# Kernel optimization log

Measured on AMD Instinct MI355X. Metric: run time of the kernel, lower is better.

## Reference

```python
import jax, jax.numpy as jnp
import numpy as np

B, S, D, H = 2, 2048, 1024, 16
DK = D // H

def setup_inputs() -> dict:
    key = jax.random.key(0)
    ks = jax.random.split(key, 12)
    scale = 1.0 / np.sqrt(D)
    inp = {
        'q': jax.random.normal(ks[0], (B, S, D), jnp.float32),
        'k': jax.random.normal(ks[1], (B, S, D), jnp.float32),
        'v': jax.random.normal(ks[2], (B, S, D), jnp.float32),
        # causal mask: 1 where attending is allowed (j <= i), 0 for future tokens
        'mask': jnp.tril(jnp.ones((S, S), jnp.int32))[None, None, :, :],
        'wq': jax.random.normal(ks[3], (D, D), jnp.float32) * scale,
        'bq': jnp.zeros((D,), jnp.float32),
        'wk': jax.random.normal(ks[4], (D, D), jnp.float32) * scale,
        'bk': jnp.zeros((D,), jnp.float32),
        'wv': jax.random.normal(ks[5], (D, D), jnp.float32) * scale,
        'bv': jnp.zeros((D,), jnp.float32),
        'wo': jax.random.normal(ks[6], (D, D), jnp.float32) * scale,
        'bo': jnp.zeros((D,), jnp.float32),
    }
    return inp


def reference(q, k, v, mask, wq, bq, wk, bk, wv, bv, wo, bo):
    def split_heads(x):
        # [B,S,D] -> [B,H,S,DK]
        return x.reshape(B, S, H, DK).transpose(0, 2, 1, 3)

    query = split_heads(q @ wq + bq)
    key_ = split_heads(k @ wk + bk)
    value = split_heads(v @ wv + bv)

    # [B,H,S,S] attention scores
    scores = jnp.einsum('bhqd,bhkd->bhqk', query, key_) / jnp.sqrt(
        jnp.asarray(DK, jnp.float32))
    scores = jnp.where(mask == 0, jnp.asarray(-1e9, scores.dtype), scores)
    attn = jax.nn.softmax(scores, axis=-1)  # dropout p=0.0 (eval mode)

    x = jnp.einsum('bhqk,bhkd->bhqd', attn, value)  # [B,H,S,DK]
    x = x.transpose(0, 2, 1, 3).reshape(B, S, D)
    return x @ wo + bo
```

## Files before the change

### kernel.cpp

```cpp
#include <hip/hip_runtime.h>
#include <hip/hip_bf16.h>

#define BATCH 2
#define SEQ   2048
#define DMODEL 1024
#define NHEAD 16
#define DK    64
#define MTOK  (BATCH * SEQ)

typedef __attribute__((ext_vector_type(8))) short bf16x8;
typedef __attribute__((ext_vector_type(4))) float f32x4;

__device__ __forceinline__ unsigned short f2bf(float x) {
    unsigned u = __float_as_uint(x);
    u = (u + 0x7FFFu + ((u >> 16) & 1u)) >> 16;
    return (unsigned short)u;
}

__device__ __forceinline__ void store_out(float* p, float v)          { *p = v; }
__device__ __forceinline__ void store_out(unsigned short* p, float v) { *p = f2bf(v); }

__device__ __forceinline__ void g2lds16(const void* g, void* l) {
    __builtin_amdgcn_global_load_lds(
        (const __attribute__((address_space(1))) void*)g,
        (__attribute__((address_space(3))) void*)l, 16, 0, 0);
}

template <int N>
__device__ __forceinline__ void s_wait_vmcnt() {
    asm volatile("s_waitcnt vmcnt(%0)" :: "n"(N) : "memory");
}
__device__ __forceinline__ void s_wait_lgkm0() {
    asm volatile("s_waitcnt lgkmcnt(0)" ::: "memory");
}
__device__ __forceinline__ void s_bar() {
    asm volatile("s_barrier" ::: "memory");
}

__global__ __launch_bounds__(256) void cvt3_bf16_kernel(
    const float* __restrict__ s0, const float* __restrict__ s1,
    const float* __restrict__ s2,
    unsigned short* __restrict__ d0, unsigned short* __restrict__ d1,
    unsigned short* __restrict__ d2, int n)
{
    const float* src; unsigned short* dst;
    switch (blockIdx.z) {
        case 0:  src = s0; dst = d0; break;
        case 1:  src = s1; dst = d1; break;
        default: src = s2; dst = d2; break;
    }
    int i = (blockIdx.x * 256 + threadIdx.x) * 8;
    if (i >= n) return;
    float4 a = *(const float4*)(src + i);
    float4 b = *(const float4*)(src + i + 4);
    union { unsigned short s[8]; uint4 u; } o;
    o.s[0] = f2bf(a.x); o.s[1] = f2bf(a.y); o.s[2] = f2bf(a.z); o.s[3] = f2bf(a.w);
    o.s[4] = f2bf(b.x); o.s[5] = f2bf(b.y); o.s[6] = f2bf(b.z); o.s[7] = f2bf(b.w);
    *(uint4*)(dst + i) = o.u;
}

__global__ __launch_bounds__(256) void wtrans_kernel(
    const float* __restrict__ w0, const float* __restrict__ w1,
    const float* __restrict__ w2, const float* __restrict__ w3,
    unsigned short* __restrict__ t0, unsigned short* __restrict__ t1,
    unsigned short* __restrict__ t2, unsigned short* __restrict__ t3)
{
    __shared__ float tile[32][33];
    const float* W; unsigned short* T;
    switch (blockIdx.z) {
        case 0:  W = w0; T = t0; break;
        case 1:  W = w1; T = t1; break;
        case 2:  W = w2; T = t2; break;
        default: W = w3; T = t3; break;
    }
    const int n0 = blockIdx.x * 32, k0 = blockIdx.y * 32;
    const int t  = threadIdx.x;
    const int r  = t >> 3;
    const int c4 = (t & 7) * 4;

    float4 v = *(const float4*)&W[(size_t)(k0 + r) * DMODEL + n0 + c4];
    tile[r][c4 + 0] = v.x; tile[r][c4 + 1] = v.y;
    tile[r][c4 + 2] = v.z; tile[r][c4 + 3] = v.w;
    __syncthreads();

    union { unsigned short s[4]; uint2 u; } o;
#pragma unroll
    for (int u = 0; u < 4; ++u) o.s[u] = f2bf(tile[c4 + u][r]);
    *(uint2*)&T[(size_t)(n0 + r) * DMODEL + k0 + c4] = o.u;
}

struct GemmP {
    const unsigned short* A;
    const unsigned short* Bt;
    const float* bias;
    void* C;
    int N, K, ctShift, biasByRow;
    float scale;
};
struct Gemm3 { GemmP p[3]; };

template <typename OutT, int NC>
__global__ __launch_bounds__(512, 2) void gemm_lds_kernel(Gemm3 g)
{
    constexpr int NCW   = NC / 4;
    constexpr int NBLK  = 32 + 2 * NC;
    constexpr int PW    = NBLK / 8;
    constexpr int BUFSZ = NBLK * 512;

    __shared__ unsigned short sS[2 * BUFSZ];

    const unsigned nx  = gridDim.x;
    const unsigned lin = blockIdx.x + nx * blockIdx.z;
    const unsigned ch  = (nx * gridDim.z) >> 3;
    const unsigned l2  = (lin & 7u) * ch + (lin >> 3);
    const unsigned zz  = l2 / nx;
    const unsigned bid = l2 - zz * nx;

    const GemmP p = g.p[zz];
    const unsigned short* __restrict__ A  = p.A;
    const unsigned short* __restrict__ Bt = p.Bt;
    OutT* __restrict__ C = (OutT*)p.C;
    const int K = p.K, N = p.N;

    const int bx = (int)(bid & ((1u << p.ctShift) - 1u));
    const int by = (int)(bid >> p.ctShift);
    const int row0 = by * 256;
    const int col0 = bx * (NC * 16);

    const int t    = threadIdx.x;
    const int w    = t >> 6;
    const int lane = t & 63;
    const int ln   = lane & 15;
    const int qg   = lane >> 4;
    const int wm   = w >> 2;
    const int wn   = w & 3;

    const unsigned short* sp[PW];
    int lo[PW];
#pragma unroll
    for (int i = 0; i < PW; ++i) {
        const int s = w * PW + i;
        if (s < 32) {
            const int mtg = s >> 1, kc = s & 1;
            sp[i] = A + (size_t)(row0 + mtg * 16 + ln) * K + kc * 32 + qg * 8;
        } else {
            const int bi = s - 32;
            const int ntg = bi >> 1, kc = bi & 1;
            sp[i] = Bt + (size_t)(col0 + ntg * 16 + ln) * K + kc * 32 + qg * 8;
        }
        lo[i] = s * 512;
    }

    f32x4 acc[8][NCW];
#pragma unroll
    for (int mt = 0; mt < 8; ++mt)
#pragma unroll
        for (int nt = 0; nt < NCW; ++nt) acc[mt][nt] = (f32x4){0.f, 0.f, 0.f, 0.f};

    const int NT = K / 64;

#pragma unroll
    for (int i = 0; i < PW; ++i) g2lds16(sp[i], &sS[lo[i]]);
#pragma unroll
    for (int i = 0; i < PW; ++i) g2lds16(sp[i] + 64, &sS[BUFSZ + lo[i]]);

    int curOff = 0;
    for (int kt = 0; kt < NT; ++kt) {
        if (kt < NT - 1) s_wait_vmcnt<PW>();
        else             s_wait_vmcnt<0>();
        s_bar();

        const unsigned short* bufA = &sS[curOff];
        const unsigned short* bufB = &sS[curOff + 32 * 512];
#pragma unroll
        for (int kc = 0; kc < 2; ++kc) {
            bf16x8 aF[8], bF[NCW];
#pragma unroll
            for (int mt = 0; mt < 8; ++mt)
                aF[mt] = *(const bf16x8*)&bufA[(((wm * 8 + mt) * 2) + kc) * 512 + lane * 8];
#pragma unroll
            for (int n2 = 0; n2 < NCW; ++n2)
                bF[n2] = *(const bf16x8*)&bufB[(((wn * NCW + n2) * 2) + kc) * 512 + lane * 8];
#pragma unroll
            for (int mt = 0; mt < 8; ++mt)
#pragma unroll
                for (int n2 = 0; n2 < NCW; ++n2)
                    acc[mt][n2] = __builtin_amdgcn_mfma_f32_16x16x32_bf16(
                        aF[mt], bF[n2], acc[mt][n2], 0, 0, 0);
        }

        s_wait_lgkm0();
        s_bar();

        if (kt + 2 < NT) {
            const int koff = (kt + 2) * 64;
#pragma unroll
            for (int i = 0; i < PW; ++i)
                g2lds16(sp[i] + koff, &sS[curOff + lo[i]]);
        }
        curOff ^= BUFSZ;
    }

    float bcol[NCW], brow[8][4];
    if (!p.biasByRow) {
#pragma unroll
        for (int n2 = 0; n2 < NCW; ++n2)
            bcol[n2] = p.bias[col0 + (wn * NCW + n2) * 16 + ln];
    } else {
#pragma unroll
        for (int mt = 0; mt < 8; ++mt)
#pragma unroll
            for (int r = 0; r < 4; ++r)
                brow[mt][r] = p.bias[row0 + wm * 128 + mt * 16 + qg * 4 + r];
    }

#pragma unroll
    for (int mt = 0; mt < 8; ++mt)
#pragma unroll
        for (int n2 = 0; n2 < NCW; ++n2)
#pragma unroll
            for (int r = 0; r < 4; ++r) {
                int row = row0 + wm * 128 + mt * 16 + qg * 4 + r;
                int col = col0 + (wn * NCW + n2) * 16 + ln;
                float bb = p.biasByRow ? brow[mt][r] : bcol[n2];
                store_out(&C[(size_t)row * N + col], (acc[mt][n2][r] + bb) * p.scale);
            }
}

#define BR 64
#define BC 64
#define PSTR 72

__global__ __launch_bounds__(256) void attn_mfma_kernel(
    const unsigned short* __restrict__ Qg, const unsigned short* __restrict__ Kg,
    const unsigned short* __restrict__ VT, unsigned short* __restrict__ O)
{
    __shared__ unsigned short sK[2][8 * 512];
    __shared__ unsigned short sV[2][8 * 512];
    __shared__ unsigned short sQ[8 * 512];
    __shared__ unsigned short sP[BR * PSTR];

    const int t    = threadIdx.x;
    const int w    = t >> 6;
    const int lane = t & 63;
    const int ln   = lane & 15;
    const int qg   = lane >> 4;

    const int id  = blockIdx.x;
    const int bh  = id & 31;
    const int qt  = (SEQ / BR - 1) - (id >> 5);
    const int b   = bh >> 4;
    const int h   = bh & 15;
    const int qi0 = qt * BR;

    const size_t rowbase = (size_t)b * SEQ;
    const size_t colbase = (size_t)h * DK;

#pragma unroll
    for (int i = 0; i < 2; ++i) {
        const int s = w * 2 + i;
        const int nt = s >> 1, kc = s & 1;
        g2lds16(Qg + (rowbase + qi0 + w * 16 + ln) * DMODEL + colbase + i * 32 + qg * 8,
                &sQ[s * 512]);
        g2lds16(Kg + (rowbase + nt * 16 + ln) * DMODEL + colbase + kc * 32 + qg * 8,
                &sK[0][s * 512]);
        g2lds16(VT + (size_t)(colbase + nt * 16 + ln) * MTOK + rowbase + kc * 32 + qg * 8,
                &sV[0][s * 512]);
    }
    __syncthreads();

    bf16x8 aq[2];
#pragma unroll
    for (int kc = 0; kc < 2; ++kc)
        aq[kc] = *(const bf16x8*)&sQ[(w * 2 + kc) * 512 + lane * 8];

    const short one_bf = (short)0x3F80;
    const bf16x8 bone = (bf16x8){one_bf, one_bf, one_bf, one_bf,
                                 one_bf, one_bf, one_bf, one_bf};

    f32x4 ofrag[4];
#pragma unroll
    for (int nt = 0; nt < 4; ++nt) ofrag[nt] = (f32x4){0.f, 0.f, 0.f, 0.f};
    f32x4 osum = (f32x4){0.f, 0.f, 0.f, 0.f};
    float m_r[4];
#pragma unroll
    for (int r = 0; r < 4; ++r) m_r[r] = -3.0e38f;

    const int ntiles = qt + 1;
    for (int jt = 0; jt < ntiles; ++jt) {
        const int cur = jt & 1;

        if (jt + 1 < ntiles) {
            const int j1 = (jt + 1) * BC;
            const int nb = cur ^ 1;
#pragma unroll
            for (int i = 0; i < 2; ++i) {
                const int s = w * 2 + i;
                const int nt = s >> 1, kc = s & 1;
                g2lds16(Kg + (rowbase + j1 + nt * 16 + ln) * DMODEL + colbase + kc * 32 + qg * 8,
                        &sK[nb][s * 512]);
                g2lds16(VT + (size_t)(colbase + nt * 16 + ln) * MTOK + rowbase + j1 + kc * 32 + qg * 8,
                        &sV[nb][s * 512]);
            }
        }

        f32x4 sf[4];
#pragma unroll
        for (int nt = 0; nt < 4; ++nt) {
            f32x4 a2 = (f32x4){0.f, 0.f, 0.f, 0.f};
#pragma unroll
            for (int kc = 0; kc < 2; ++kc) {
                bf16x8 bk = *(const bf16x8*)&sK[cur][(nt * 2 + kc) * 512 + lane * 8];
                a2 = __builtin_amdgcn_mfma_f32_16x16x32_bf16(aq[kc], bk, a2, 0, 0, 0);
            }
            sf[nt] = a2;
        }

        if (jt == ntiles - 1) {
#pragma unroll
            for (int nt = 0; nt < 4; ++nt)
#pragma unroll
                for (int r = 0; r < 4; ++r) {
                    int qrow = w * 16 + qg * 4 + r;
                    int col  = nt * 16 + ln;
                    if (col > qrow) sf[nt][r] = -1.0e30f;
                }
        }

        float rmax[4];
#pragma unroll
        for (int r = 0; r < 4; ++r)
            rmax[r] = fmaxf(fmaxf(sf[0][r], sf[1][r]), fmaxf(sf[2][r], sf[3][r]));
#pragma unroll
        for (int off = 8; off >= 1; off >>= 1)
#pragma unroll
            for (int r = 0; r < 4; ++r)
                rmax[r] = fmaxf(rmax[r], __shfl_xor(rmax[r], off));

        float alpha[4];
#pragma unroll
        for (int r = 0; r < 4; ++r) {
            float mn = fmaxf(m_r[r], rmax[r]);
            alpha[r] = exp2f(m_r[r] - mn);
            m_r[r] = mn;
        }

#pragma unroll
        for (int nt = 0; nt < 4; ++nt)
#pragma unroll
            for (int r = 0; r < 4; ++r) {
                float pv = exp2f(sf[nt][r] - m_r[r]);
                int row = w * 16 + qg * 4 + r;
                int col = (nt * 16 + ln) ^ (((w * 4 + qg) & 7) * 8);
                sP[row * PSTR + col] = f2bf(pv);
            }

#pragma unroll
        for (int nt = 0; nt < 4; ++nt)
#pragma unroll
            for (int r = 0; r < 4; ++r) ofrag[nt][r] *= alpha[r];
#pragma unroll
        for (int r = 0; r < 4; ++r) osum[r] *= alpha[r];

        bf16x8 apf[2];
#pragma unroll
        for (int kc = 0; kc < 2; ++kc) {
            int row = w * 16 + ln;
            int col = (kc * 32 + qg * 8) ^ ((((row >> 2) & 7)) * 8);
            apf[kc] = *(const bf16x8*)&sP[row * PSTR + col];
        }

#pragma unroll
        for (int kc = 0; kc < 2; ++kc)
            osum = __builtin_amdgcn_mfma_f32_16x16x32_bf16(apf[kc], bone, osum, 0, 0, 0);
#pragma unroll
        for (int nt = 0; nt < 4; ++nt) {
#pragma unroll
            for (int kc = 0; kc < 2; ++kc) {
                bf16x8 bv = *(const bf16x8*)&sV[cur][(nt * 2 + kc) * 512 + lane * 8];
                ofrag[nt] = __builtin_amdgcn_mfma_f32_16x16x32_bf16(apf[kc], bv, ofrag[nt], 0, 0, 0);
            }
        }

        __syncthreads();
    }

    float inv[4];
#pragma unroll
    for (int r = 0; r < 4; ++r) inv[r] = 1.0f / osum[r];
#pragma unroll
    for (int nt = 0; nt < 4; ++nt)
#pragma unroll
        for (int r = 0; r < 4; ++r) {
            int gq = qi0 + w * 16 + qg * 4 + r;
            O[(rowbase + gq) * DMODEL + colbase + nt * 16 + ln] =
                f2bf(ofrag[nt][r] * inv[r]);
        }
}

extern "C" void kernel_launch(void* const* d_in, const int* in_sizes, int n_in,
                              void* d_out, int out_size, void* d_ws, size_t ws_size,
                              hipStream_t stream)
{
    const float* q  = (const float*)d_in[0];
    const float* k  = (const float*)d_in[1];
    const float* v  = (const float*)d_in[2];
    const float* wq = (const float*)d_in[4];
    const float* bq = (const float*)d_in[5];
    const float* wk = (const float*)d_in[6];
    const float* bk = (const float*)d_in[7];
    const float* wv = (const float*)d_in[8];
    const float* bv = (const float*)d_in[9];
    const float* wo = (const float*)d_in[10];
    const float* bo = (const float*)d_in[11];
    float* out = (float*)d_out;

    const size_t mat  = (size_t)MTOK * DMODEL;
    const size_t wmat = (size_t)DMODEL * DMODEL;
    unsigned short* Abq = (unsigned short*)d_ws;
    unsigned short* Abk = Abq + mat;
    unsigned short* Abv = Abk + mat;
    unsigned short* WtQ = Abv + mat;
    unsigned short* WtK = WtQ + wmat;
    unsigned short* WtV = WtK + wmat;
    unsigned short* WtO = WtV + wmat;
    unsigned short* Qb  = WtO + wmat;
    unsigned short* Kb  = Qb + mat;
    unsigned short* VT  = Kb + mat;
    unsigned short* CTX = VT + mat;

    cvt3_bf16_kernel<<<dim3((unsigned)(mat / 2048), 1, 3), 256, 0, stream>>>(
        q, k, v, Abq, Abk, Abv, (int)mat);
    wtrans_kernel<<<dim3(32, 32, 4), 256, 0, stream>>>(wq, wk, wv, wo, WtQ, WtK, WtV, WtO);

    const float qscale = 0.125f * 1.44269504088896f;
    Gemm3 g;
    g.p[0] = (GemmP){Abq, WtQ, bq, (void*)Qb, DMODEL, DMODEL, 2, 0, qscale};
    g.p[1] = (GemmP){Abk, WtK, bk, (void*)Kb, DMODEL, DMODEL, 2, 0, 1.0f};
    g.p[2] = (GemmP){WtV, Abv, bv, (void*)VT, MTOK,   DMODEL, 4, 1, 1.0f};
    gemm_lds_kernel<unsigned short, 16><<<dim3(64, 1, 3), 512, 0, stream>>>(g);

    attn_mfma_kernel<<<BATCH * NHEAD * (SEQ / BR), 256, 0, stream>>>(Qb, Kb, VT, CTX);

    Gemm3 go;
    go.p[0] = (GemmP){CTX, WtO, bo, (void*)out, DMODEL, DMODEL, 3, 0, 1.0f};
    go.p[1] = go.p[0];
    go.p[2] = go.p[0];
    gemm_lds_kernel<float, 8><<<dim3(128, 1, 1), 512, 0, stream>>>(go);
}
```

Before: 270.4 us.

## Compute transposed scores to keep P in registers; shrink output GEMM tile

The attention kernel now computes S^T by swapping MFMA operands, so each lane holds a key-column slice for one query row. Row max and sum reduce with two cross-group shuffles, and the P tile is repacked into MFMA A-operand layout with cross-lane shuffles and packed bf16 converts. This removes the shared-memory P buffer, its write/read round trip and the ones-vector MFMA that computed row sums. Separately, the GEMM template gains an M-tile parameter, and the output projection uses 128x128 tiles with 256 blocks to fill more compute units, at the cost of more operand reloads.

Result: faster. 257.1 us (-4.9%).

```diff
diff --git a/kernel.cpp b/kernel.cpp
--- a/kernel.cpp
+++ b/kernel.cpp
@@ -19,6 +19,12 @@
 
 __device__ __forceinline__ void store_out(float* p, float v)          { *p = v; }
 __device__ __forceinline__ void store_out(unsigned short* p, float v) { *p = f2bf(v); }
+
+__device__ __forceinline__ unsigned cvt_pk_bf16(float x, float y) {
+    unsigned d;
+    asm("v_cvt_pk_bf16_f32 %0, %1, %2" : "=v"(d) : "v"(x), "v"(y));
+    return d;
+}
 
 __device__ __forceinline__ void g2lds16(const void* g, void* l) {
     __builtin_amdgcn_global_load_lds(
@@ -99,11 +105,12 @@
 };
 struct Gemm3 { GemmP p[3]; };
 
-template <typename OutT, int NC>
+template <typename OutT, int MR, int NC>
 __global__ __launch_bounds__(512, 2) void gemm_lds_kernel(Gemm3 g)
 {
+    constexpr int AM    = MR / 2;
     constexpr int NCW   = NC / 4;
-    constexpr int NBLK  = 32 + 2 * NC;
+    constexpr int NBLK  = 2 * MR + 2 * NC;
     constexpr int PW    = NBLK / 8;
     constexpr int BUFSZ = NBLK * 512;
 
@@ -124,7 +131,7 @@
 
     const int bx = (int)(bid & ((1u << p.ctShift) - 1u));
     const int by = (int)(bid >> p.ctShift);
-    const int row0 = by * 256;
+    const int row0 = by * (MR * 16);
     const int col0 = bx * (NC * 16);
 
     const int t    = threadIdx.x;
@@ -140,20 +147,20 @@
 #pragma unroll
     for (int i = 0; i < PW; ++i) {
         const int s = w * PW + i;
-        if (s < 32) {
+        if (s < 2 * MR) {
             const int mtg = s >> 1, kc = s & 1;
             sp[i] = A + (size_t)(row0 + mtg * 16 + ln) * K + kc * 32 + qg * 8;
         } else {
-            const int bi = s - 32;
+            const int bi = s - 2 * MR;
             const int ntg = bi >> 1, kc = bi & 1;
             sp[i] = Bt + (size_t)(col0 + ntg * 16 + ln) * K + kc * 32 + qg * 8;
         }
         lo[i] = s * 512;
     }
 
-    f32x4 acc[8][NCW];
-#pragma unroll
-    for (int mt = 0; mt < 8; ++mt)
+    f32x4 acc[AM][NCW];
+#pragma unroll
+    for (int mt = 0; mt < AM; ++mt)
 #pragma unroll
         for (int nt = 0; nt < NCW; ++nt) acc[mt][nt] = (f32x4){0.f, 0.f, 0.f, 0.f};
 
@@ -171,18 +178,18 @@
         s_bar();
 
         const unsigned short* bufA = &sS[curOff];
-        const unsigned short* bufB = &sS[curOff + 32 * 512];
+        const unsigned short* bufB = &sS[curOff + 2 * MR * 512];
 #pragma unroll
         for (int kc = 0; kc < 2; ++kc) {
-            bf16x8 aF[8], bF[NCW];
-#pragma unroll
-            for (int mt = 0; mt < 8; ++mt)
-                aF[mt] = *(const bf16x8*)&bufA[(((wm * 8 + mt) * 2) + kc) * 512 + lane * 8];
+            bf16x8 aF[AM], bF[NCW];
+#pragma unroll
+            for (int mt = 0; mt < AM; ++mt)
+                aF[mt] = *(const bf16x8*)&bufA[(((wm * AM + mt) * 2) + kc) * 512 + lane * 8];
 #pragma unroll
             for (int n2 = 0; n2 < NCW; ++n2)
                 bF[n2] = *(const bf16x8*)&bufB[(((wn * NCW + n2) * 2) + kc) * 512 + lane * 8];
 #pragma unroll
-            for (int mt = 0; mt < 8; ++mt)
+            for (int mt = 0; mt < AM; ++mt)
 #pragma unroll
                 for (int n2 = 0; n2 < NCW; ++n2)
                     acc[mt][n2] = __builtin_amdgcn_mfma_f32_16x16x32_bf16(
@@ -201,26 +208,26 @@
         curOff ^= BUFSZ;
     }
 
-    float bcol[NCW], brow[8][4];
+    float bcol[NCW], brow[AM][4];
     if (!p.biasByRow) {
 #pragma unroll
         for (int n2 = 0; n2 < NCW; ++n2)
             bcol[n2] = p.bias[col0 + (wn * NCW + n2) * 16 + ln];
     } else {
 #pragma unroll
-        for (int mt = 0; mt < 8; ++mt)
+        for (int mt = 0; mt < AM; ++mt)
 #pragma unroll
             for (int r = 0; r < 4; ++r)
-                brow[mt][r] = p.bias[row0 + wm * 128 + mt * 16 + qg * 4 + r];
-    }
-
-#pragma unroll
-    for (int mt = 0; mt < 8; ++mt)
+                brow[mt][r] = p.bias[row0 + wm * (AM * 16) + mt * 16 + qg * 4 + r];
+    }
+
+#pragma unroll
+    for (int mt = 0; mt < AM; ++mt)
 #pragma unroll
         for (int n2 = 0; n2 < NCW; ++n2)
 #pragma unroll
             for (int r = 0; r < 4; ++r) {
-                int row = row0 + wm * 128 + mt * 16 + qg * 4 + r;
+                int row = row0 + wm * (AM * 16) + mt * 16 + qg * 4 + r;
                 int col = col0 + (wn * NCW + n2) * 16 + ln;
                 float bb = p.biasByRow ? brow[mt][r] : bcol[n2];
                 store_out(&C[(size_t)row * N + col], (acc[mt][n2][r] + bb) * p.scale);
@@ -229,7 +236,6 @@
 
 #define BR 64
 #define BC 64
-#define PSTR 72
 
 __global__ __launch_bounds__(256) void attn_mfma_kernel(
     const unsigned short* __restrict__ Qg, const unsigned short* __restrict__ Kg,
@@ -238,7 +244,6 @@
     __shared__ unsigned short sK[2][8 * 512];
     __shared__ unsigned short sV[2][8 * 512];
     __shared__ unsigned short sQ[8 * 512];
-    __shared__ unsigned short sP[BR * PSTR];
 
     const int t    = threadIdx.x;
     const int w    = t >> 6;
@@ -274,17 +279,15 @@
     for (int kc = 0; kc < 2; ++kc)
         aq[kc] = *(const bf16x8*)&sQ[(w * 2 + kc) * 512 + lane * 8];
 
-    const short one_bf = (short)0x3F80;
-    const bf16x8 bone = (bf16x8){one_bf, one_bf, one_bf, one_bf,
-                                 one_bf, one_bf, one_bf, one_bf};
-
     f32x4 ofrag[4];
 #pragma unroll
     for (int nt = 0; nt < 4; ++nt) ofrag[nt] = (f32x4){0.f, 0.f, 0.f, 0.f};
-    f32x4 osum = (f32x4){0.f, 0.f, 0.f, 0.f};
-    float m_r[4];
-#pragma unroll
-    for (int r = 0; r < 4; ++r) m_r[r] = -3.0e38f;
+    float osum_p = 0.f;
+    float m_run  = -3.0e38f;
+
+    const int laneA = ((2 * qg) & 3) * 16 + ln;
+    const int laneB = ((2 * qg + 1) & 3) * 16 + ln;
+    const bool hiSel = (qg >> 1) & 1;
 
     const int ntiles = qt + 1;
     for (int jt = 0; jt < ntiles; ++jt) {
@@ -311,83 +314,99 @@
 #pragma unroll
             for (int kc = 0; kc < 2; ++kc) {
                 bf16x8 bk = *(const bf16x8*)&sK[cur][(nt * 2 + kc) * 512 + lane * 8];
-                a2 = __builtin_amdgcn_mfma_f32_16x16x32_bf16(aq[kc], bk, a2, 0, 0, 0);
+                a2 = __builtin_amdgcn_mfma_f32_16x16x32_bf16(bk, aq[kc], a2, 0, 0, 0);
             }
             sf[nt] = a2;
         }
 
         if (jt == ntiles - 1) {
+            const int qloc = w * 16 + ln;
 #pragma unroll
             for (int nt = 0; nt < 4; ++nt)
 #pragma unroll
-                for (int r = 0; r < 4; ++r) {
-                    int qrow = w * 16 + qg * 4 + r;
-                    int col  = nt * 16 + ln;
-                    if (col > qrow) sf[nt][r] = -1.0e30f;
-                }
-        }
-
-        float rmax[4];
-#pragma unroll
-        for (int r = 0; r < 4; ++r)
-            rmax[r] = fmaxf(fmaxf(sf[0][r], sf[1][r]), fmaxf(sf[2][r], sf[3][r]));
-#pragma unroll
-        for (int off = 8; off >= 1; off >>= 1)
-#pragma unroll
-            for (int r = 0; r < 4; ++r)
-                rmax[r] = fmaxf(rmax[r], __shfl_xor(rmax[r], off));
-
-        float alpha[4];
-#pragma unroll
-        for (int r = 0; r < 4; ++r) {
-            float mn = fmaxf(m_r[r], rmax[r]);
-            alpha[r] = exp2f(m_r[r] - mn);
-            m_r[r] = mn;
-        }
-
+                for (int r = 0; r < 4; ++r)
+                    if (nt * 16 + qg * 4 + r > qloc) sf[nt][r] = -1.0e30f;
+        }
+
+        float pmax = sf[0][0];
 #pragma unroll
         for (int nt = 0; nt < 4; ++nt)
 #pragma unroll
+            for (int r = 0; r < 4; ++r) pmax = fmaxf(pmax, sf[nt][r]);
+        pmax = fmaxf(pmax, __shfl_xor(pmax, 16));
+        pmax = fmaxf(pmax, __shfl_xor(pmax, 32));
+
+        const float mn = fmaxf(m_run, pmax);
+        const float al = exp2f(m_run - mn);
+        m_run = mn;
+
+        float pv[4][4];
+        float lsum = 0.f;
+#pragma unroll
+        for (int nt = 0; nt < 4; ++nt)
+#pragma unroll
             for (int r = 0; r < 4; ++r) {
-                float pv = exp2f(sf[nt][r] - m_r[r]);
-                int row = w * 16 + qg * 4 + r;
-                int col = (nt * 16 + ln) ^ (((w * 4 + qg) & 7) * 8);
-                sP[row * PSTR + col] = f2bf(pv);
+                float e = exp2f(sf[nt][r] - mn);
+                pv[nt][r] = e;
+                lsum += e;
             }
-
+        osum_p = osum_p * al + lsum;
+
+        float alr[4];
+#pragma unroll
+        for (int r = 0; r < 4; ++r) alr[r] = __shfl(al, qg * 4 + r);
 #pragma unroll
         for (int nt = 0; nt < 4; ++nt)
 #pragma unroll
-            for (int r = 0; r < 4; ++r) ofrag[nt][r] *= alpha[r];
-#pragma unroll
-        for (int r = 0; r < 4; ++r) osum[r] *= alpha[r];
-
-        bf16x8 apf[2];
-#pragma unroll
-        for (int kc = 0; kc < 2; ++kc) {
-            int row = w * 16 + ln;
-            int col = (kc * 32 + qg * 8) ^ ((((row >> 2) & 7)) * 8);
-            apf[kc] = *(const bf16x8*)&sP[row * PSTR + col];
-        }
-
-#pragma unroll
-        for (int kc = 0; kc < 2; ++kc)
-            osum = __builtin_amdgcn_mfma_f32_16x16x32_bf16(apf[kc], bone, osum, 0, 0, 0);
+            for (int r = 0; r < 4; ++r) ofrag[nt][r] *= alr[r];
+
+        unsigned pk0[2], pk1[2], pk2[2], pk3[2];
+#pragma unroll
+        for (int rr = 0; rr < 2; ++rr) {
+            pk0[rr] = cvt_pk_bf16(pv[0][2 * rr], pv[0][2 * rr + 1]);
+            pk1[rr] = cvt_pk_bf16(pv[1][2 * rr], pv[1][2 * rr + 1]);
+            pk2[rr] = cvt_pk_bf16(pv[2][2 * rr], pv[2][2 * rr + 1]);
+            pk3[rr] = cvt_pk_bf16(pv[3][2 * rr], pv[3][2 * rr + 1]);
+        }
+        union { bf16x8 v; unsigned u[4]; } ap[2];
+        {
+            unsigned s0, s1;
+            s0 = (unsigned)__shfl((int)pk0[0], laneA); s1 = (unsigned)__shfl((int)pk1[0], laneA);
+            ap[0].u[0] = hiSel ? s1 : s0;
+            s0 = (unsigned)__shfl((int)pk0[1], laneA); s1 = (unsigned)__shfl((int)pk1[1], laneA);
+            ap[0].u[1] = hiSel ? s1 : s0;
+            s0 = (unsigned)__shfl((int)pk0[0], laneB); s1 = (unsigned)__shfl((int)pk1[0], laneB);
+            ap[0].u[2] = hiSel ? s1 : s0;
+            s0 = (unsigned)__shfl((int)pk0[1], laneB); s1 = (unsigned)__shfl((int)pk1[1], laneB);
+            ap[0].u[3] = hiSel ? s1 : s0;
+            s0 = (unsigned)__shfl((int)pk2[0], laneA); s1 = (unsigned)__shfl((int)pk3[0], laneA);
+            ap[1].u[0] = hiSel ? s1 : s0;
+            s0 = (unsigned)__shfl((int)pk2[1], laneA); s1 = (unsigned)__shfl((int)pk3[1], laneA);
+            ap[1].u[1] = hiSel ? s1 : s0;
+            s0 = (unsigned)__shfl((int)pk2[0], laneB); s1 = (unsigned)__shfl((int)pk3[0], laneB);
+            ap[1].u[2] = hiSel ? s1 : s0;
+            s0 = (unsigned)__shfl((int)pk2[1], laneB); s1 = (unsigned)__shfl((int)pk3[1], laneB);
+            ap[1].u[3] = hiSel ? s1 : s0;
+        }
+
 #pragma unroll
         for (int nt = 0; nt < 4; ++nt) {
 #pragma unroll
             for (int kc = 0; kc < 2; ++kc) {
                 bf16x8 bv = *(const bf16x8*)&sV[cur][(nt * 2 + kc) * 512 + lane * 8];
-                ofrag[nt] = __builtin_amdgcn_mfma_f32_16x16x32_bf16(apf[kc], bv, ofrag[nt], 0, 0, 0);
+                ofrag[nt] = __builtin_amdgcn_mfma_f32_16x16x32_bf16(ap[kc].v, bv, ofrag[nt], 0, 0, 0);
             }
         }
 
         __syncthreads();
     }
 
+    float osum = osum_p + __shfl_xor(osum_p, 16);
+    osum += __shfl_xor(osum, 32);
+    const float invq = 1.0f / osum;
     float inv[4];
 #pragma unroll
-    for (int r = 0; r < 4; ++r) inv[r] = 1.0f / osum[r];
+    for (int r = 0; r < 4; ++r) inv[r] = __shfl(invq, qg * 4 + r);
 #pragma unroll
     for (int nt = 0; nt < 4; ++nt)
 #pragma unroll
@@ -438,7 +457,7 @@
     g.p[0] = (GemmP){Abq, WtQ, bq, (void*)Qb, DMODEL, DMODEL, 2, 0, qscale};
     g.p[1] = (GemmP){Abk, WtK, bk, (void*)Kb, DMODEL, DMODEL, 2, 0, 1.0f};
     g.p[2] = (GemmP){WtV, Abv, bv, (void*)VT, MTOK,   DMODEL, 4, 1, 1.0f};
-    gemm_lds_kernel<unsigned short, 16><<<dim3(64, 1, 3), 512, 0, stream>>>(g);
+    gemm_lds_kernel<unsigned short, 16, 16><<<dim3(64, 1, 3), 512, 0, stream>>>(g);
 
     attn_mfma_kernel<<<BATCH * NHEAD * (SEQ / BR), 256, 0, stream>>>(Qb, Kb, VT, CTX);
 
@@ -446,5 +465,5 @@
     go.p[0] = (GemmP){CTX, WtO, bo, (void*)out, DMODEL, DMODEL, 3, 0, 1.0f};
     go.p[1] = go.p[0];
     go.p[2] = go.p[0];
-    gemm_lds_kernel<float, 8><<<dim3(128, 1, 1), 512, 0, stream>>>(go);
-}
+    gemm_lds_kernel<float, 8, 8><<<dim3(256, 1, 1), 512, 0, stream>>>(go);
+}
```
